# Kernel optimization log

Measured on AMD Instinct MI355X. Metric: run time of the kernel, lower is better.

Reference implementation:

```python
import jax, jax.numpy as jnp
import numpy as np

N_NODES = 50000


def setup_inputs() -> dict:
    key = jax.random.key(0)
    k1, k2, k3, k4 = jax.random.split(key, 4)
    x = jax.random.normal(k1, (N_NODES, 256), dtype=jnp.float32)
    edge_index = jax.random.randint(k2, (2, 800000), 0, N_NODES, dtype=jnp.int64)
    W1 = jax.random.normal(k3, (256, 128), dtype=jnp.float32) * (1.0 / np.sqrt(256))
    b1 = jnp.zeros((128,), dtype=jnp.float32)
    W2 = jax.random.normal(k4, (128, 16), dtype=jnp.float32) * (1.0 / np.sqrt(128))
    b2 = jnp.zeros((16,), dtype=jnp.float32)
    return {"x": x, "edge_index": edge_index, "W1": W1, "b1": b1, "W2": W2, "b2": b2}


def _gcn_norm(edge_index, num_nodes):
    # add self-loops, then symmetric normalization D^-1/2 A D^-1/2 (PyG GCNConv default)
    loop = jnp.arange(num_nodes, dtype=edge_index.dtype)
    src = jnp.concatenate([edge_index[0], loop])
    dst = jnp.concatenate([edge_index[1], loop])
    deg = jax.ops.segment_sum(jnp.ones_like(dst, dtype=jnp.float32), dst, num_segments=num_nodes)
    dinv = jnp.where(deg > 0, jax.lax.rsqrt(deg), 0.0)
    norm = dinv[src] * dinv[dst]  # [E+N]
    return src, dst, norm


def _gcn_conv(h, W, b, src, dst, norm, num_nodes):
    h = h @ W                             # linear before propagate
    msg = h[src] * norm[:, None]          # gather + edge scaling
    agg = jax.ops.segment_sum(msg, dst, num_segments=num_nodes)  # scatter-add
    return agg + b


def reference(x, edge_index, W1, b1, W2, b2):
    n = x.shape[0]
    src, dst, norm = _gcn_norm(edge_index, n)
    h = jax.nn.relu(_gcn_conv(x, W1, b1, src, dst, norm, n))
    # F.dropout(training=False) is identity in eval mode
    out = _gcn_conv(h, W2, b2, src, dst, norm, n)
    return jax.nn.log_softmax(out, axis=1)
```

## Files before the change

kernel.cpp:

```cpp
#include <hip/hip_runtime.h>
#include <hip/hip_bf16.h>
#include <math.h>


#define FIN 256
#define FH  128
#define FO  16
#define ECH_LOG 13
#define ECH (1 << ECH_LOG)
#define NCHUNK 98
#define WPH 6272

typedef unsigned int uint;
typedef unsigned short ushort;
typedef unsigned char uchar;
typedef __attribute__((ext_vector_type(8))) short bf16x8;
typedef __attribute__((ext_vector_type(4))) float f32x4;

static __device__ __forceinline__ ushort f2bf(float f) {
    __hip_bfloat16 b = __float2bfloat16(f);
    return *reinterpret_cast<ushort*>(&b);
}
static __device__ __forceinline__ float bf2f(ushort u) {
    return __uint_as_float(((uint)u) << 16);
}

__global__ __launch_bounds__(256) void GCN_histwprep_k(
        const int* __restrict__ edge, uint* __restrict__ cw,
        uchar* __restrict__ rank8,
        const float* __restrict__ W1, ushort* __restrict__ whT,
        ushort* __restrict__ wlT,
        int E, int nHist, int nWords, int wph) {
    __shared__ uint lh[WPH];
    int tid = threadIdx.x;

    if ((int)blockIdx.x >= nHist) {
        int i = (blockIdx.x - nHist) * 256 + tid;
        int k = i >> 7, c = i & 127;
        float w = W1[i];
        ushort hh = f2bf(w);
        ushort hl = f2bf(w - bf2f(hh));
        whT[c * 256 + k] = hh;
        wlT[c * 256 + k] = hl;
        return;
    }

    int bid = blockIdx.x;
    int half = bid & 1;
    int c = bid >> 1;
    int w0 = half * wph;
    int wlim = nWords - w0; if (wlim > wph) wlim = wph;
    for (int j = tid; j < wlim; j += 256) lh[j] = 0;
    __syncthreads();
    int base = c << ECH_LOG;
    int lim = base + ECH; if (lim > E) lim = E;
    for (int i = base + tid; i < lim; i += 256) {
        int d = edge[E + i];
        int wd = (d >> 2) - w0;
        if ((unsigned)wd < (unsigned)wlim) {
            int sh = (d & 3) << 3;
            uint old = atomicAdd(&lh[wd], 1u << sh);
            rank8[i] = (uchar)((old >> sh) & 0xFFu);
        }
    }
    __syncthreads();
    for (int j = tid; j < wlim; j += 256)
        cw[(size_t)c * nWords + w0 + j] = lh[j];
}

__global__ __launch_bounds__(256) void GCN_chpfx_k(uint* __restrict__ cw,
                                                   int* __restrict__ count,
                                                   int* __restrict__ bsum,
                                                   int N, int nWords) {
    __shared__ int part[4][64][4];
    __shared__ int red[64];
    int tid = threadIdx.x;
    int wl = tid & 63, g = tid >> 6;
    int w = blockIdx.x * 64 + wl;
    int c0 = g * 25;
    int c1 = c0 + 25; if (c1 > NCHUNK) c1 = NCHUNK;

    int s0 = 0, s1 = 0, s2 = 0, s3 = 0;
    if (w < nWords) {
        for (int c = c0; c < c1; c++) {
            uint v = cw[(size_t)c * nWords + w];
            s0 += (int)(v & 0xFFu);
            s1 += (int)((v >> 8) & 0xFFu);
            s2 += (int)((v >> 16) & 0xFFu);
            s3 += (int)((v >> 24) & 0xFFu);
        }
    }
    part[g][wl][0] = s0; part[g][wl][1] = s1;
    part[g][wl][2] = s2; part[g][wl][3] = s3;
    __syncthreads();

    int b0 = 0, b1 = 0, b2 = 0, b3 = 0;
    for (int gg = 0; gg < g; gg++) {
        b0 += part[gg][wl][0]; b1 += part[gg][wl][1];
        b2 += part[gg][wl][2]; b3 += part[gg][wl][3];
    }
    if (w < nWords) {
        uint r0 = (uint)b0, r1 = (uint)b1, r2 = (uint)b2, r3 = (uint)b3;
        for (int c = c0; c < c1; c++) {
            uint* p = &cw[(size_t)c * nWords + w];
            uint v = *p;
            *p = (r0 & 0xFFu) | ((r1 & 0xFFu) << 8) | ((r2 & 0xFFu) << 16) | ((r3 & 0xFFu) << 24);
            r0 += v & 0xFFu;
            r1 += (v >> 8) & 0xFFu;
            r2 += (v >> 16) & 0xFFu;
            r3 += (v >> 24) & 0xFFu;
        }
    }
    int local = 0;
    if (g == 3 && w < nWords) {
        int t0 = b0 + s0, t1 = b1 + s1, t2 = b2 + s2, t3 = b3 + s3;
        int d0 = 4 * w;
        if (d0 + 0 < N) count[d0 + 0] = t0;
        if (d0 + 1 < N) count[d0 + 1] = t1;
        if (d0 + 2 < N) count[d0 + 2] = t2;
        if (d0 + 3 < N) count[d0 + 3] = t3;
        local = t0 + t1 + t2 + t3 + 4;
    }
    if (g == 3) red[wl] = local;
    __syncthreads();
    if (tid < 32) { red[tid] += red[tid + 32]; }
    __syncthreads();
    if (tid < 16) { red[tid] += red[tid + 16]; }
    __syncthreads();
    if (tid < 8) { red[tid] += red[tid + 8]; }
    __syncthreads();
    if (tid < 4) { red[tid] += red[tid + 4]; }
    __syncthreads();
    if (tid == 0) bsum[blockIdx.x] = red[0] + red[1] + red[2] + red[3];
}

__global__ __launch_bounds__(256) void GCN_scan2_k(const int* __restrict__ count,
                                                   const int* __restrict__ bsum,
                                                   int2* __restrict__ rd2,
                                                   uint* __restrict__ edata, int N) {
    int tid = threadIdx.x;
    int b = blockIdx.x;
    int d = b * 256 + tid;
    int cnt1 = (d < N) ? count[d] + 1 : 0;

    __shared__ int red[256];
    int offp = 0;
    for (int t = tid; t < b; t += 256) offp += bsum[t];
    red[tid] = offp;
    __syncthreads();
    for (int st = 128; st > 0; st >>= 1) {
        if (tid < st) red[tid] += red[tid + st];
        __syncthreads();
    }
    int blockOff = red[0];
    __syncthreads();

    __shared__ int ssum[256];
    ssum[tid] = cnt1;
    __syncthreads();
    for (int off = 1; off < 256; off <<= 1) {
        int t = (tid >= off) ? ssum[tid - off] : 0;
        __syncthreads();
        ssum[tid] += t;
        __syncthreads();
    }
    int r = blockOff + ssum[tid] - cnt1;

    if (d < N) {
        float dv = rsqrtf((float)cnt1);
        rd2[d] = make_int2(r, __float_as_int(dv));
        edata[r] = (uint)d | ((uint)f2bf(dv * dv) << 16);
    }
    if (b == gridDim.x - 1 && tid == 255) rd2[N] = make_int2(blockOff + ssum[255], 0);
}

#define G1_BR 64
#define G1_KC 32

__global__ __launch_bounds__(256, 4) void GCN_fillgemm_k(
        const int* __restrict__ edge, const uchar* __restrict__ rank8,
        const uint* __restrict__ cw, const int2* __restrict__ rd2,
        uint* __restrict__ edata,
        const float* __restrict__ x, const ushort* __restrict__ whT,
        const ushort* __restrict__ wlT, ushort* __restrict__ h1,
        int N, int E, int nFill, int nWords) {
    __shared__ __align__(16) char smem[20480];
    int tid = threadIdx.x;

    if ((int)blockIdx.x < nFill) {
        int i = blockIdx.x * 256 + tid;
        if (i < E) {
            int s = edge[i];
            int d = edge[E + i];
            int rk = (int)rank8[i];
            int c = i >> ECH_LOG;
            uint pw = cw[(size_t)c * nWords + (d >> 2)];
            int pfx = (int)((pw >> ((d & 3) << 3)) & 0xFFu);
            int2 rdd = rd2[d];
            float ds = __int_as_float(rd2[s].y);
            float nr = ds * __int_as_float(rdd.y);
            edata[rdd.x + 1 + pfx + rk] = (uint)s | ((uint)f2bf(nr) << 16);
        }
        return;
    }

    ushort* xh_s = (ushort*)smem;
    ushort* wh_s = (ushort*)(smem + 4096);
    ushort* wl_s = (ushort*)(smem + 12288);
    int row0 = (blockIdx.x - nFill) * G1_BR;
    int ln = tid & 63;
    int w  = tid >> 6;
    int ln15 = ln & 15;
    int q16  = ln >> 4;

    f32x4 acc[4][2];
    #pragma unroll
    for (int mr = 0; mr < 4; mr++)
        #pragma unroll
        for (int nc = 0; nc < 2; nc++) acc[mr][nc] = (f32x4){0.f, 0.f, 0.f, 0.f};

    for (int kc = 0; kc < FIN; kc += G1_KC) {
        #pragma unroll
        for (int j = 0; j < 2; j++) {
            int u = tid + j * 256;
            int r = u >> 3, kq = u & 7;
            int gr = row0 + r;
            float4 v = make_float4(0.f, 0.f, 0.f, 0.f);
            if (gr < N) v = *(const float4*)&x[(size_t)gr * FIN + kc + kq * 4];
            uint2 hw;
            hw.x = (uint)f2bf(v.x) | ((uint)f2bf(v.y) << 16);
            hw.y = (uint)f2bf(v.z) | ((uint)f2bf(v.w) << 16);
            int byte = (r * 64 + kq * 8) ^ (((r >> 1) & 3) << 4);
            *(uint2*)((char*)xh_s + byte) = hw;
        }
        #pragma unroll
        for (int j = 0; j < 2; j++) {
            int u = tid + j * 256;
            int c = u >> 2, ku = u & 3;
            uint4 vh = *(const uint4*)&whT[(size_t)c * 256 + kc + ku * 8];
            uint4 vl = *(const uint4*)&wlT[(size_t)c * 256 + kc + ku * 8];
            int byte = (c * 64 + ku * 16) ^ (((c >> 1) & 3) << 4);
            *(uint4*)((char*)wh_s + byte) = vh;
            *(uint4*)((char*)wl_s + byte) = vl;
        }
        __syncthreads();

        bf16x8 ah[4], bh[2], bl[2];
        #pragma unroll
        for (int mr = 0; mr < 4; mr++) {
            int r = mr * 16 + ln15;
            int byte = r * 64 + ((q16 * 16) ^ (((r >> 1) & 3) << 4));
            ah[mr] = *(const bf16x8*)((const char*)xh_s + byte);
        }
        #pragma unroll
        for (int nc = 0; nc < 2; nc++) {
            int c = w * 32 + nc * 16 + ln15;
            int byte = c * 64 + ((q16 * 16) ^ (((c >> 1) & 3) << 4));
            bh[nc] = *(const bf16x8*)((const char*)wh_s + byte);
            bl[nc] = *(const bf16x8*)((const char*)wl_s + byte);
        }
        #pragma unroll
        for (int mr = 0; mr < 4; mr++)
            #pragma unroll
            for (int nc = 0; nc < 2; nc++) {
                acc[mr][nc] = __builtin_amdgcn_mfma_f32_16x16x32_bf16(
                    ah[mr], bh[nc], acc[mr][nc], 0, 0, 0);
                acc[mr][nc] = __builtin_amdgcn_mfma_f32_16x16x32_bf16(
                    ah[mr], bl[nc], acc[mr][nc], 0, 0, 0);
            }
        __syncthreads();
    }

    #pragma unroll
    for (int mr = 0; mr < 4; mr++) {
        #pragma unroll
        for (int nc = 0; nc < 2; nc++) {
            int cw2 = w * 32 + nc * 16 + ln15;
            #pragma unroll
            for (int j = 0; j < 4; j++) {
                int gr = row0 + mr * 16 + q16 * 4 + j;
                if (gr < N) h1[(size_t)gr * FH + cw2] = f2bf(acc[mr][nc][j]);
            }
        }
    }
}

__global__ __launch_bounds__(256) void GCN_agg1gemm2_k(
        const ushort* __restrict__ h1, const int2* __restrict__ rd2,
        const uint* __restrict__ ed, const float* __restrict__ b1,
        const float* __restrict__ W2, ushort* __restrict__ h2b, int N) {
    __shared__ float w2s[FH][FO];
    __shared__ float hs[16][FH + 4];
    int tid = threadIdx.x;
    #pragma unroll
    for (int j = 0; j < (FH * FO) / 256; j++) {
        int i = tid + j * 256;
        w2s[i >> 4][i & 15] = W2[i];
    }

    int node0 = blockIdx.x * 16;
    int local = tid >> 4;
    int j = tid & 15;
    int node = node0 + local;

    if (node < N) {
        int beg = rd2[node].x, end = rd2[node + 1].x;
        const uint4* hp = (const uint4*)h1;

        float a[8];
        #pragma unroll
        for (int t = 0; t < 8; t++) a[t] = 0.f;

        int i = beg;
        for (; i + 8 <= end; i += 8) {
            uint e[8];
            uint4 gg[8];
            #pragma unroll
            for (int t = 0; t < 8; t++) e[t] = ed[i + t];
            #pragma unroll
            for (int t = 0; t < 8; t++) gg[t] = hp[(size_t)(e[t] & 0xFFFFu) * 16 + j];
            #pragma unroll
            for (int t = 0; t < 8; t++) {
                float w = bf2f((ushort)(e[t] >> 16));
                #pragma unroll
                for (int q = 0; q < 4; q++) {
                    uint u = (&gg[t].x)[q];
                    a[q*2+0] += __uint_as_float(u << 16) * w;
                    a[q*2+1] += __uint_as_float(u & 0xFFFF0000u) * w;
                }
            }
        }
        for (; i < end; i++) {
            uint e = ed[i];
            float w = bf2f((ushort)(e >> 16));
            uint4 g = hp[(size_t)(e & 0xFFFFu) * 16 + j];
            #pragma unroll
            for (int q = 0; q < 4; q++) {
                uint u = (&g.x)[q];
                a[q*2+0] += __uint_as_float(u << 16) * w;
                a[q*2+1] += __uint_as_float(u & 0xFFFF0000u) * w;
            }
        }

        const float4* bp = (const float4*)b1;
        float4 bb0 = bp[j * 2 + 0];
        float4 bb1 = bp[j * 2 + 1];
        float4 o0, o1;
        o0.x = fmaxf(a[0] + bb0.x, 0.f);
        o0.y = fmaxf(a[1] + bb0.y, 0.f);
        o0.z = fmaxf(a[2] + bb0.z, 0.f);
        o0.w = fmaxf(a[3] + bb0.w, 0.f);
        o1.x = fmaxf(a[4] + bb1.x, 0.f);
        o1.y = fmaxf(a[5] + bb1.y, 0.f);
        o1.z = fmaxf(a[6] + bb1.z, 0.f);
        o1.w = fmaxf(a[7] + bb1.w, 0.f);
        *(float4*)&hs[local][j * 8 + 0] = o0;
        *(float4*)&hs[local][j * 8 + 4] = o1;
    }
    __syncthreads();

    float acc = 0.f;
    #pragma unroll 8
    for (int k = 0; k < FH; k++) acc += hs[local][k] * w2s[k][j];
    if (node < N) h2b[(size_t)node * FO + j] = f2bf(acc);
}

__global__ __launch_bounds__(256) void GCN_agg2_k(const ushort* __restrict__ h2b,
                                                  const int2* __restrict__ rd2,
                                                  const uint* __restrict__ ed,
                                                  const float* __restrict__ b2,
                                                  float* __restrict__ out, int N) {
    int tid = threadIdx.x;
    int node = blockIdx.x * 32 + (tid >> 3);
    if (node >= N) return;
    int f2 = tid & 7;
    int beg = rd2[node].x, end = rd2[node + 1].x;
    const uint* hp = (const uint*)h2b;
    float a0 = 0.f, a1 = 0.f;
    int i = beg;
    for (; i + 8 <= end; i += 8) {
        uint e[8];
        uint u[8];
        #pragma unroll
        for (int t = 0; t < 8; t++) e[t] = ed[i + t];
        #pragma unroll
        for (int t = 0; t < 8; t++) u[t] = hp[(size_t)(e[t] & 0xFFFFu) * 8 + f2];
        #pragma unroll
        for (int t = 0; t < 8; t++) {
            float w = bf2f((ushort)(e[t] >> 16));
            a0 += __uint_as_float(u[t] << 16) * w;
            a1 += __uint_as_float(u[t] & 0xFFFF0000u) * w;
        }
    }
    for (; i < end; i++) {
        uint e = ed[i];
        uint u = hp[(size_t)(e & 0xFFFFu) * 8 + f2];
        float w = bf2f((ushort)(e >> 16));
        a0 += __uint_as_float(u << 16) * w;
        a1 += __uint_as_float(u & 0xFFFF0000u) * w;
    }
    float2 bb = ((const float2*)b2)[f2];
    float v0 = a0 + bb.x;
    float v1 = a1 + bb.y;
    float mx = fmaxf(v0, v1);
    #pragma unroll
    for (int m = 4; m >= 1; m >>= 1) mx = fmaxf(mx, __shfl_xor(mx, m, 8));
    float s = expf(v0 - mx) + expf(v1 - mx);
    #pragma unroll
    for (int m = 4; m >= 1; m >>= 1) s += __shfl_xor(s, m, 8);
    float ls = logf(s);
    float2 o = make_float2(v0 - mx - ls, v1 - mx - ls);
    ((float2*)out)[(size_t)node * 8 + f2] = o;
}

extern "C" void kernel_launch(void* const* d_in, const int* in_sizes, int n_in,
                              void* d_out, int out_size, void* d_ws, size_t ws_size,
                              hipStream_t stream) {
    (void)n_in; (void)out_size; (void)ws_size;
    const float* x  = (const float*)d_in[0];
    const int*   edp = (const int*)d_in[1];
    const float* W1 = (const float*)d_in[2];
    const float* b1 = (const float*)d_in[3];
    const float* W2 = (const float*)d_in[4];
    const float* b2 = (const float*)d_in[5];
    float* out = (float*)d_out;

    int N = in_sizes[0] / FIN;
    int E = in_sizes[1] / 2;
    int M = E + N;
    int nWords = (N + 3) / 4;
    int wph = (nWords + 1) / 2;
    int nScanBlocks = (N + 255) / 256;
    int nChpfx = (nWords + 63) / 64;

    char* p = (char*)d_ws;
    auto take = [&](size_t bytes) -> char* {
        char* r = p;
        p += (bytes + 255) & ~(size_t)255;
        return r;
    };
    int*    count  = (int*)take((size_t)N * 4);
    uchar*  rank8  = (uchar*)take((size_t)E);
    uint*   cw     = (uint*)take((size_t)NCHUNK * nWords * 4);
    int2*   rd2    = (int2*)take((size_t)(N + 1) * 8);
    int*    bsum   = (int*)take((size_t)nChpfx * 4);
    uint*   edata  = (uint*)take((size_t)M * 4);
    ushort* whT    = (ushort*)take((size_t)FH * FIN * 2);
    ushort* wlT    = (ushort*)take((size_t)FH * FIN * 2);
    ushort* h1     = (ushort*)take((size_t)N * FH * 2);
    ushort* h2b    = (ushort*)take((size_t)N * FO * 2);

    int eBlocks = (E + 255) / 256;
    int nGemm   = (N + G1_BR - 1) / G1_BR;
    int nHist   = 2 * NCHUNK;

    GCN_histwprep_k<<<nHist + (FIN * FH) / 256, 256, 0, stream>>>(
        edp, cw, rank8, W1, whT, wlT, E, nHist, nWords, wph);
    GCN_chpfx_k<<<nChpfx, 256, 0, stream>>>(cw, count, bsum, N, nWords);
    GCN_scan2_k<<<nScanBlocks, 256, 0, stream>>>(count, bsum, rd2, edata, N);
    GCN_fillgemm_k<<<eBlocks + nGemm, 256, 0, stream>>>(
        edp, rank8, cw, rd2, edata, x, whT, wlT, h1, N, E, eBlocks, nWords);
    GCN_agg1gemm2_k<<<(N + 15) / 16, 256, 0, stream>>>(h1, rd2, edata, b1, W2, h2b, N);
    GCN_agg2_k<<<(N + 31) / 32, 256, 0, stream>>>(h2b, rd2, edata, b2, out, N);
}
```

Measured before the change: 119.1 us.

## Co-schedule GEMM1 with histogram kernel and split fill into its own launch

Moves the first dense GEMM (x·W1 with split-bf16 weights) out of the fill kernel and into the histogram kernel, so it overlaps the LDS-atomic histogram work instead of the scatter fill. Weight preparation becomes its own small kernel launched first, and the fill becomes a standalone kernel. The histogram/GEMM kernel now reserves a larger shared-memory array (sized for the histogram), which can lower occupancy for the GEMM blocks. It also adds one extra kernel launch overall.

```diff
diff --git a/kernel.cpp b/kernel.cpp
--- a/kernel.cpp
+++ b/kernel.cpp
@@ -25,47 +25,135 @@
     return __uint_as_float(((uint)u) << 16);
 }
 
-__global__ __launch_bounds__(256) void GCN_histwprep_k(
+__global__ __launch_bounds__(256) void GCN_wprep_k(const float* __restrict__ W1,
+                                                   ushort* __restrict__ whT,
+                                                   ushort* __restrict__ wlT) {
+    int i = blockIdx.x * 256 + threadIdx.x;
+    int k = i >> 7, c = i & 127;
+    float w = W1[i];
+    ushort hh = f2bf(w);
+    ushort hl = f2bf(w - bf2f(hh));
+    whT[c * 256 + k] = hh;
+    wlT[c * 256 + k] = hl;
+}
+
+#define G1_BR 64
+#define G1_KC 32
+
+__global__ __launch_bounds__(256, 4) void GCN_histgemm_k(
+        const float* __restrict__ x, const ushort* __restrict__ whT,
+        const ushort* __restrict__ wlT, ushort* __restrict__ h1,
         const int* __restrict__ edge, uint* __restrict__ cw,
         uchar* __restrict__ rank8,
-        const float* __restrict__ W1, ushort* __restrict__ whT,
-        ushort* __restrict__ wlT,
-        int E, int nHist, int nWords, int wph) {
-    __shared__ uint lh[WPH];
+        int N, int E, int nHist, int nWords, int wph) {
+    __shared__ __align__(16) char smem[WPH * 4];
     int tid = threadIdx.x;
 
-    if ((int)blockIdx.x >= nHist) {
-        int i = (blockIdx.x - nHist) * 256 + tid;
-        int k = i >> 7, c = i & 127;
-        float w = W1[i];
-        ushort hh = f2bf(w);
-        ushort hl = f2bf(w - bf2f(hh));
-        whT[c * 256 + k] = hh;
-        wlT[c * 256 + k] = hl;
+    if ((int)blockIdx.x < nHist) {
+        int bid = blockIdx.x;
+        int half = bid & 1;
+        int c = bid >> 1;
+        uint* lh = (uint*)smem;
+        int w0 = half * wph;
+        int wlim = nWords - w0; if (wlim > wph) wlim = wph;
+        for (int j = tid; j < wlim; j += 256) lh[j] = 0;
+        __syncthreads();
+        int base = c << ECH_LOG;
+        int lim = base + ECH; if (lim > E) lim = E;
+        for (int i = base + tid; i < lim; i += 256) {
+            int d = edge[E + i];
+            int wd = (d >> 2) - w0;
+            if ((unsigned)wd < (unsigned)wlim) {
+                int sh = (d & 3) << 3;
+                uint old = atomicAdd(&lh[wd], 1u << sh);
+                rank8[i] = (uchar)((old >> sh) & 0xFFu);
+            }
+        }
+        __syncthreads();
+        for (int j = tid; j < wlim; j += 256)
+            cw[(size_t)c * nWords + w0 + j] = lh[j];
         return;
     }
 
-    int bid = blockIdx.x;
-    int half = bid & 1;
-    int c = bid >> 1;
-    int w0 = half * wph;
-    int wlim = nWords - w0; if (wlim > wph) wlim = wph;
-    for (int j = tid; j < wlim; j += 256) lh[j] = 0;
-    __syncthreads();
-    int base = c << ECH_LOG;
-    int lim = base + ECH; if (lim > E) lim = E;
-    for (int i = base + tid; i < lim; i += 256) {
-        int d = edge[E + i];
-        int wd = (d >> 2) - w0;
-        if ((unsigned)wd < (unsigned)wlim) {
-            int sh = (d & 3) << 3;
-            uint old = atomicAdd(&lh[wd], 1u << sh);
-            rank8[i] = (uchar)((old >> sh) & 0xFFu);
-        }
-    }
-    __syncthreads();
-    for (int j = tid; j < wlim; j += 256)
-        cw[(size_t)c * nWords + w0 + j] = lh[j];
+    ushort* xh_s = (ushort*)smem;
+    ushort* wh_s = (ushort*)(smem + 4096);
+    ushort* wl_s = (ushort*)(smem + 12288);
+    int row0 = (blockIdx.x - nHist) * G1_BR;
+    int ln = tid & 63;
+    int w  = tid >> 6;
+    int ln15 = ln & 15;
+    int q16  = ln >> 4;
+
+    f32x4 acc[4][2];
+    #pragma unroll
+    for (int mr = 0; mr < 4; mr++)
+        #pragma unroll
+        for (int nc = 0; nc < 2; nc++) acc[mr][nc] = (f32x4){0.f, 0.f, 0.f, 0.f};
+
+    for (int kc = 0; kc < FIN; kc += G1_KC) {
+        #pragma unroll
+        for (int j = 0; j < 2; j++) {
+            int u = tid + j * 256;
+            int r = u >> 3, kq = u & 7;
+            int gr = row0 + r;
+            float4 v = make_float4(0.f, 0.f, 0.f, 0.f);
+            if (gr < N) v = *(const float4*)&x[(size_t)gr * FIN + kc + kq * 4];
+            uint2 hw;
+            hw.x = (uint)f2bf(v.x) | ((uint)f2bf(v.y) << 16);
+            hw.y = (uint)f2bf(v.z) | ((uint)f2bf(v.w) << 16);
+            int byte = (r * 64 + kq * 8) ^ (((r >> 1) & 3) << 4);
+            *(uint2*)((char*)xh_s + byte) = hw;
+        }
+        #pragma unroll
+        for (int j = 0; j < 2; j++) {
+            int u = tid + j * 256;
+            int c = u >> 2, ku = u & 3;
+            uint4 vh = *(const uint4*)&whT[(size_t)c * 256 + kc + ku * 8];
+            uint4 vl = *(const uint4*)&wlT[(size_t)c * 256 + kc + ku * 8];
+            int byte = (c * 64 + ku * 16) ^ (((c >> 1) & 3) << 4);
+            *(uint4*)((char*)wh_s + byte) = vh;
+            *(uint4*)((char*)wl_s + byte) = vl;
+        }
+        __syncthreads();
+
+        bf16x8 ah[4], bh[2], bl[2];
+        #pragma unroll
+        for (int mr = 0; mr < 4; mr++) {
+            int r = mr * 16 + ln15;
+            int byte = r * 64 + ((q16 * 16) ^ (((r >> 1) & 3) << 4));
+            ah[mr] = *(const bf16x8*)((const char*)xh_s + byte);
+        }
+        #pragma unroll
+        for (int nc = 0; nc < 2; nc++) {
+            int c = w * 32 + nc * 16 + ln15;
+            int byte = c * 64 + ((q16 * 16) ^ (((c >> 1) & 3) << 4));
+            bh[nc] = *(const bf16x8*)((const char*)wh_s + byte);
+            bl[nc] = *(const bf16x8*)((const char*)wl_s + byte);
+        }
+        #pragma unroll
+        for (int mr = 0; mr < 4; mr++)
+            #pragma unroll
+            for (int nc = 0; nc < 2; nc++) {
+                acc[mr][nc] = __builtin_amdgcn_mfma_f32_16x16x32_bf16(
+                    ah[mr], bh[nc], acc[mr][nc], 0, 0, 0);
+                acc[mr][nc] = __builtin_amdgcn_mfma_f32_16x16x32_bf16(
+                    ah[mr], bl[nc], acc[mr][nc], 0, 0, 0);
+            }
+        __syncthreads();
+    }
+
+    #pragma unroll
+    for (int mr = 0; mr < 4; mr++) {
+        #pragma unroll
+        for (int nc = 0; nc < 2; nc++) {
+            int cw2 = w * 32 + nc * 16 + ln15;
+            #pragma unroll
+            for (int j = 0; j < 4; j++) {
+                int gr = row0 + mr * 16 + q16 * 4 + j;
+                if (gr < N) h1[(size_t)gr * FH + cw2] = f2bf(acc[mr][nc][j]);
+            }
+        }
+    }
 }
 
 __global__ __launch_bounds__(256) void GCN_chpfx_k(uint* __restrict__ cw,
@@ -174,115 +262,24 @@
     if (b == gridDim.x - 1 && tid == 255) rd2[N] = make_int2(blockOff + ssum[255], 0);
 }
 
-#define G1_BR 64
-#define G1_KC 32
-
-__global__ __launch_bounds__(256, 4) void GCN_fillgemm_k(
-        const int* __restrict__ edge, const uchar* __restrict__ rank8,
-        const uint* __restrict__ cw, const int2* __restrict__ rd2,
-        uint* __restrict__ edata,
-        const float* __restrict__ x, const ushort* __restrict__ whT,
-        const ushort* __restrict__ wlT, ushort* __restrict__ h1,
-        int N, int E, int nFill, int nWords) {
-    __shared__ __align__(16) char smem[20480];
-    int tid = threadIdx.x;
-
-    if ((int)blockIdx.x < nFill) {
-        int i = blockIdx.x * 256 + tid;
-        if (i < E) {
-            int s = edge[i];
-            int d = edge[E + i];
-            int rk = (int)rank8[i];
-            int c = i >> ECH_LOG;
-            uint pw = cw[(size_t)c * nWords + (d >> 2)];
-            int pfx = (int)((pw >> ((d & 3) << 3)) & 0xFFu);
-            int2 rdd = rd2[d];
-            float ds = __int_as_float(rd2[s].y);
-            float nr = ds * __int_as_float(rdd.y);
-            edata[rdd.x + 1 + pfx + rk] = (uint)s | ((uint)f2bf(nr) << 16);
-        }
-        return;
-    }
-
-    ushort* xh_s = (ushort*)smem;
-    ushort* wh_s = (ushort*)(smem + 4096);
-    ushort* wl_s = (ushort*)(smem + 12288);
-    int row0 = (blockIdx.x - nFill) * G1_BR;
-    int ln = tid & 63;
-    int w  = tid >> 6;
-    int ln15 = ln & 15;
-    int q16  = ln >> 4;
-
-    f32x4 acc[4][2];
-    #pragma unroll
-    for (int mr = 0; mr < 4; mr++)
-        #pragma unroll
-        for (int nc = 0; nc < 2; nc++) acc[mr][nc] = (f32x4){0.f, 0.f, 0.f, 0.f};
-
-    for (int kc = 0; kc < FIN; kc += G1_KC) {
-        #pragma unroll
-        for (int j = 0; j < 2; j++) {
-            int u = tid + j * 256;
-            int r = u >> 3, kq = u & 7;
-            int gr = row0 + r;
-            float4 v = make_float4(0.f, 0.f, 0.f, 0.f);
-            if (gr < N) v = *(const float4*)&x[(size_t)gr * FIN + kc + kq * 4];
-            uint2 hw;
-            hw.x = (uint)f2bf(v.x) | ((uint)f2bf(v.y) << 16);
-            hw.y = (uint)f2bf(v.z) | ((uint)f2bf(v.w) << 16);
-            int byte = (r * 64 + kq * 8) ^ (((r >> 1) & 3) << 4);
-            *(uint2*)((char*)xh_s + byte) = hw;
-        }
-        #pragma unroll
-        for (int j = 0; j < 2; j++) {
-            int u = tid + j * 256;
-            int c = u >> 2, ku = u & 3;
-            uint4 vh = *(const uint4*)&whT[(size_t)c * 256 + kc + ku * 8];
-            uint4 vl = *(const uint4*)&wlT[(size_t)c * 256 + kc + ku * 8];
-            int byte = (c * 64 + ku * 16) ^ (((c >> 1) & 3) << 4);
-            *(uint4*)((char*)wh_s + byte) = vh;
-            *(uint4*)((char*)wl_s + byte) = vl;
-        }
-        __syncthreads();
-
-        bf16x8 ah[4], bh[2], bl[2];
-        #pragma unroll
-        for (int mr = 0; mr < 4; mr++) {
-            int r = mr * 16 + ln15;
-            int byte = r * 64 + ((q16 * 16) ^ (((r >> 1) & 3) << 4));
-            ah[mr] = *(const bf16x8*)((const char*)xh_s + byte);
-        }
-        #pragma unroll
-        for (int nc = 0; nc < 2; nc++) {
-            int c = w * 32 + nc * 16 + ln15;
-            int byte = c * 64 + ((q16 * 16) ^ (((c >> 1) & 3) << 4));
-            bh[nc] = *(const bf16x8*)((const char*)wh_s + byte);
-            bl[nc] = *(const bf16x8*)((const char*)wl_s + byte);
-        }
-        #pragma unroll
-        for (int mr = 0; mr < 4; mr++)
-            #pragma unroll
-            for (int nc = 0; nc < 2; nc++) {
-                acc[mr][nc] = __builtin_amdgcn_mfma_f32_16x16x32_bf16(
-                    ah[mr], bh[nc], acc[mr][nc], 0, 0, 0);
-                acc[mr][nc] = __builtin_amdgcn_mfma_f32_16x16x32_bf16(
-                    ah[mr], bl[nc], acc[mr][nc], 0, 0, 0);
-            }
-        __syncthreads();
-    }
-
-    #pragma unroll
-    for (int mr = 0; mr < 4; mr++) {
-        #pragma unroll
-        for (int nc = 0; nc < 2; nc++) {
-            int cw2 = w * 32 + nc * 16 + ln15;
-            #pragma unroll
-            for (int j = 0; j < 4; j++) {
-                int gr = row0 + mr * 16 + q16 * 4 + j;
-                if (gr < N) h1[(size_t)gr * FH + cw2] = f2bf(acc[mr][nc][j]);
-            }
-        }
-    }
+__global__ __launch_bounds__(256) void GCN_fill_k(const int* __restrict__ edge,
+                                                  const uchar* __restrict__ rank8,
+                                                  const uint* __restrict__ cw,
+                                                  const int2* __restrict__ rd2,
+                                                  uint* __restrict__ edata,
+                                                  int E, int nWords) {
+    int i = blockIdx.x * 256 + threadIdx.x;
+    if (i >= E) return;
+    int s = edge[i];
+    int d = edge[E + i];
+    int rk = (int)rank8[i];
+    int c = i >> ECH_LOG;
+    uint pw = cw[(size_t)c * nWords + (d >> 2)];
+    int pfx = (int)((pw >> ((d & 3) << 3)) & 0xFFu);
+    int2 rdd = rd2[d];
+    float ds = __int_as_float(rd2[s].y);
+    float nr = ds * __int_as_float(rdd.y);
+    edata[rdd.x + 1 + pfx + rk] = (uint)s | ((uint)f2bf(nr) << 16);
 }
 
 __global__ __launch_bounds__(256) void GCN_agg1gemm2_k(
@@ -454,12 +451,12 @@
     int nGemm   = (N + G1_BR - 1) / G1_BR;
     int nHist   = 2 * NCHUNK;
 
-    GCN_histwprep_k<<<nHist + (FIN * FH) / 256, 256, 0, stream>>>(
-        edp, cw, rank8, W1, whT, wlT, E, nHist, nWords, wph);
+    GCN_wprep_k<<<(FIN * FH) / 256, 256, 0, stream>>>(W1, whT, wlT);
+    GCN_histgemm_k<<<nHist + nGemm, 256, 0, stream>>>(
+        x, whT, wlT, h1, edp, cw, rank8, N, E, nHist, nWords, wph);
     GCN_chpfx_k<<<nChpfx, 256, 0, stream>>>(cw, count, bsum, N, nWords);
     GCN_scan2_k<<<nScanBlocks, 256, 0, stream>>>(count, bsum, rd2, edata, N);
-    GCN_fillgemm_k<<<eBlocks + nGemm, 256, 0, stream>>>(
-        edp, rank8, cw, rd2, edata, x, whT, wlT, h1, N, E, eBlocks, nWords);
+    GCN_fill_k<<<eBlocks, 256, 0, stream>>>(edp, rank8, cw, rd2, edata, E, nWords);
     GCN_agg1gemm2_k<<<(N + 15) / 16, 256, 0, stream>>>(h1, rd2, edata, b1, W2, h2b, N);
     GCN_agg2_k<<<(N + 31) / 32, 256, 0, stream>>>(h2b, rd2, edata, b2, out, N);
 }
```

Measured after the change: 113.1 us. 1.05x faster.
